# Optimization experiments

Measured on AMD Instinct MI355X. Metric: run time of the kernel, lower is better.

## Reference

```python
import jax, jax.numpy as jnp
import numpy as np
from jax import lax

K = 3
PAD = 1
STRIDE = 1


def setup_inputs() -> dict:
    key = jax.random.key(0)
    k1, k2, k3 = jax.random.split(key, 3)
    B, Cin, Cout, H, W = 4, 64, 64, 128, 128
    x = jax.random.normal(k1, (B, Cin, H, W), dtype=jnp.float32)
    # offset-generating conv weight: [2*K*K, Cin, K, K]
    w_offset = jax.random.normal(k2, (2 * K * K, Cin, K, K), dtype=jnp.float32) * 0.05
    # deformable conv weight: [Cout, Cin, K, K]
    w_deform = jax.random.normal(k3, (Cout, Cin, K, K), dtype=jnp.float32) * 0.05
    return {"x": x, "w_offset": w_offset, "w_deform": w_deform}


def _bilinear_sample_one(img, ys, xs):
    # img: [C, H, W]; ys, xs: [K2, Ho, Wo] float sampling coords
    H, W = img.shape[1], img.shape[2]
    y0 = jnp.floor(ys)
    x0 = jnp.floor(xs)
    wy = ys - y0  # frac weights, [K2, Ho, Wo]
    wx = xs - x0

    def gather(yi, xi):
        valid = (yi >= 0) & (yi <= H - 1) & (xi >= 0) & (xi <= W - 1)
        yc = jnp.clip(yi, 0, H - 1).astype(jnp.int32)
        xc = jnp.clip(xi, 0, W - 1).astype(jnp.int32)
        # img[:, yc, xc] -> [C, K2, Ho, Wo]; zero outside (torchvision zero-pad)
        return img[:, yc, xc] * valid[None].astype(img.dtype)

    v00 = gather(y0, x0)
    v01 = gather(y0, x0 + 1)
    v10 = gather(y0 + 1, x0)
    v11 = gather(y0 + 1, x0 + 1)
    w00 = ((1 - wy) * (1 - wx))[None]
    w01 = ((1 - wy) * wx)[None]
    w10 = (wy * (1 - wx))[None]
    w11 = (wy * wx)[None]
    return v00 * w00 + v01 * w01 + v10 * w10 + v11 * w11  # [C, K2, Ho, Wo]


def reference(x, w_offset, w_deform):
    B, Cin, H, W = x.shape
    Cout = w_deform.shape[0]
    K2 = K * K
    # 1) plain conv to produce offsets: [B, 2*K2, H, W]
    offset = lax.conv_general_dilated(
        x, w_offset, window_strides=(STRIDE, STRIDE),
        padding=((PAD, PAD), (PAD, PAD)),
        dimension_numbers=("NCHW", "OIHW", "NCHW"))
    Ho, Wo = offset.shape[2], offset.shape[3]
    # torchvision ordering: channel 2*k = dy, 2*k+1 = dx, taps row-major
    off = offset.reshape(B, K2, 2, Ho, Wo)
    dy, dx = off[:, :, 0], off[:, :, 1]  # [B, K2, Ho, Wo]
    # 2) base sampling grid per kernel tap
    kk = jnp.arange(K2)
    ki = (kk // K).astype(jnp.float32)  # tap row
    kj = (kk % K).astype(jnp.float32)   # tap col
    base_y = (jnp.arange(Ho, dtype=jnp.float32) * STRIDE - PAD)[None, :] + ki[:, None]  # [K2, Ho]
    base_x = (jnp.arange(Wo, dtype=jnp.float32) * STRIDE - PAD)[None, :] + kj[:, None]  # [K2, Wo]
    ys = base_y[None, :, :, None] + dy  # [B, K2, Ho, Wo]
    xs = base_x[None, :, None, :] + dx
    # 3) deformable bilinear gather: [B, Cin, K2, Ho, Wo]
    sampled = jax.vmap(_bilinear_sample_one)(x, ys, xs)
    # 4) weighted accumulation (the conv contraction)
    out = jnp.einsum("ock,bckhw->bohw", w_deform.reshape(Cout, Cin, K2), sampled)
    return out
```

## Files before the change

kernel.cpp:

```cpp
#include <hip/hip_runtime.h>


#define BATCH 4
#define CIN   64
#define COUT  64
#define HH    128
#define WW    128
#define HWPIX (HH*WW)

typedef __attribute__((ext_vector_type(8))) short short8;
typedef __attribute__((ext_vector_type(4))) float floatx4;

__device__ __forceinline__ unsigned short f2bf(float f) {
  unsigned int u = __float_as_uint(f);
  unsigned int r = u + 0x7fffu + ((u >> 16) & 1u);
  return (unsigned short)(r >> 16);
}
__device__ __forceinline__ float bf2f(unsigned short h) { return __uint_as_float(((unsigned int)h) << 16); }
__device__ __forceinline__ float lo16f(unsigned int u) { return __uint_as_float(u << 16); }
__device__ __forceinline__ float hi16f(unsigned int u) { return __uint_as_float(u & 0xffff0000u); }

__device__ __forceinline__ unsigned int bilin2(unsigned int u00, unsigned int u01,
                                               unsigned int u10, unsigned int u11,
                                               float w00, float w01, float w10, float w11) {
  float lo = w00 * lo16f(u00) + w01 * lo16f(u01) + w10 * lo16f(u10) + w11 * lo16f(u11);
  float hi = w00 * hi16f(u00) + w01 * hi16f(u01) + w10 * hi16f(u10) + w11 * hi16f(u11);
  unsigned int r;
  asm("v_cvt_pk_bf16_f32 %0, %1, %2" : "=v"(r) : "v"(lo), "v"(hi));
  return r;
}

__device__ __forceinline__ int swz(int a) { return a ^ (((a >> 9) & 3) << 4); }

__global__ __launch_bounds__(256) void pre_kernel(const float* __restrict__ x,
                                                  const float* __restrict__ wo,
                                                  const float* __restrict__ wd,
                                                  unsigned short* __restrict__ xThi,
                                                  unsigned short* __restrict__ xTlo,
                                                  unsigned short* __restrict__ wdA,
                                                  unsigned short* __restrict__ woAhi,
                                                  unsigned short* __restrict__ woAlo) {
  int tid = threadIdx.x;
  if (blockIdx.x < 4096) {
    __shared__ float tile[32][33];
    int t = blockIdx.x;
    int b = t >> 10, rem = t & 1023;
    int c0 = (rem >> 9) * 32, p0 = (rem & 511) * 32;
    int tx = tid & 31, ty = tid >> 5;
    const float* xb = x + (size_t)b * CIN * HWPIX;
    size_t boff = (size_t)b * HWPIX * CIN;
#pragma unroll
    for (int i = 0; i < 4; i++)
      tile[ty + i * 8][tx] = xb[(size_t)(c0 + ty + i * 8) * HWPIX + p0 + tx];
    __syncthreads();
#pragma unroll
    for (int i = 0; i < 2; i++) {
      int tt = tid + i * 256;
      int row = tt >> 4;
      int cp = tt & 15;
      float v0 = tile[cp * 2][row], v1 = tile[cp * 2 + 1][row];
      unsigned short h0 = f2bf(v0), h1 = f2bf(v1);
      unsigned short l0 = f2bf(v0 - bf2f(h0)), l1 = f2bf(v1 - bf2f(h1));
      size_t o = boff + (size_t)(p0 + row) * CIN + c0 + cp * 2;
      *(ushort2*)&xThi[o] = make_ushort2(h0, h1);
      *(ushort2*)&xTlo[o] = make_ushort2(l0, l1);
    }
  } else {
    int t = (blockIdx.x - 4096) * 256 + tid;
    if (t < 36864) {
      int j = t & 7, lane = (t >> 3) & 63, ct = (t >> 9) & 3, kc = (t >> 11) & 1, kk = t >> 12;
      int cout = ct * 16 + (lane & 15);
      int cin  = kc * 32 + (lane >> 4) * 8 + j;
      wdA[t] = f2bf(wd[(size_t)(cout * CIN + cin) * 9 + kk]);
    }
    int t2 = t - 36864;
    if (t2 >= 0 && t2 < 18432) {
      int j = t2 & 7, lane = (t2 >> 3) & 63, ct = (t2 >> 9) & 1, kc = (t2 >> 10) & 1, kk = t2 >> 11;
      int cout = ct * 16 + (lane & 15);
      int cin  = kc * 32 + (lane >> 4) * 8 + j;
      float v = (cout < 18) ? wo[(size_t)(cout * CIN + cin) * 9 + kk] : 0.f;
      unsigned short h = f2bf(v);
      woAhi[t2] = h;
      woAlo[t2] = f2bf(v - bf2f(h));
    }
  }
}

__global__ __launch_bounds__(256) void fused_dcn_kernel(const unsigned short* __restrict__ xThi,
                                                        const unsigned short* __restrict__ xTlo,
                                                        const unsigned short* __restrict__ woAhi,
                                                        const unsigned short* __restrict__ woAlo,
                                                        const unsigned short* __restrict__ wdA,
                                                        float* __restrict__ out) {
  __shared__ unsigned short sBhi2[2][4096];
  __shared__ unsigned short sBlo2[2][4096];
  __shared__ float offL[18 * 64];
  char* sHc = (char*)sBhi2;
  char* sLc = (char*)sBlo2;

  int tid = threadIdx.x;
  int hw = blockIdx.x;
  int bid = (hw & 7) * 128 + (hw >> 3);
  int b = bid >> 8, r = bid & 255, y = r >> 1, x0 = (r & 1) << 6;

  int p1 = tid >> 2, si = tid & 3;
  int lane = tid & 63, w = tid >> 6;

  const unsigned short* xhib = xThi + (size_t)b * HWPIX * CIN;
  const unsigned short* xlob = xTlo + (size_t)b * HWPIX * CIN;

  int wq = p1 >> 4, iq = p1 & 15;
  int kcd = si >> 1, qb = si & 1;
  int wb0 = ((((wq * 2 + kcd) * 64) + qb * 32 + iq) * 8) * 2;
  int wb1 = wb0 + 256;
  int swb0 = swz(wb0), swb1 = swz(wb1);
  int srb0 = swz((w * 2 + 0) * 1024 + lane * 16);
  int srb1 = swz((w * 2 + 1) * 1024 + lane * 16);

  int xp = x0 + p1;

  floatx4 oacc[2];
  oacc[0] = (floatx4){0.f, 0.f, 0.f, 0.f};
  oacc[1] = (floatx4){0.f, 0.f, 0.f, 0.f};

  auto ldA = [&](int kk, uint4& h0, uint4& h1, uint4& l0, uint4& l1) {
    int ys = y - 1 + kk / 3;
    int xs = xp - 1 + kk % 3;
    bool valid = (ys >= 0) && (ys < HH) && (xs >= 0) && (xs < WW);
    h0 = (uint4){0, 0, 0, 0}; h1 = h0; l0 = h0; l1 = h0;
    if (valid) {
      const unsigned short* ph = xhib + (size_t)(ys * WW + xs) * CIN + si * 16;
      const unsigned short* pl = xlob + (size_t)(ys * WW + xs) * CIN + si * 16;
      h0 = *(const uint4*)ph; h1 = *(const uint4*)(ph + 8);
      l0 = *(const uint4*)pl; l1 = *(const uint4*)(pl + 8);
    }
  };
  auto stageA = [&](int nxt, const uint4& h0, const uint4& h1, const uint4& l0, const uint4& l1) {
    *(uint4*)(sHc + nxt * 8192 + swb0) = h0;
    *(uint4*)(sHc + nxt * 8192 + swb1) = h1;
    *(uint4*)(sLc + nxt * 8192 + swb0) = l0;
    *(uint4*)(sLc + nxt * 8192 + swb1) = l1;
  };
  auto mfmaA = [&](int kk, int cur) {
    const short8* Ah = (const short8*)(woAhi + (size_t)kk * 2048);
    const short8* Al = (const short8*)(woAlo + (size_t)kk * 2048);
    short8 ah0a = Ah[lane],       ah1a = Ah[128 + lane];
    short8 al0a = Al[lane],       al1a = Al[128 + lane];
    short8 ah0b = Ah[64 + lane],  ah1b = Ah[192 + lane];
    short8 al0b = Al[64 + lane],  al1b = Al[192 + lane];
    short8 bh0 = *(const short8*)(sHc + cur * 8192 + srb0);
    short8 bh1 = *(const short8*)(sHc + cur * 8192 + srb1);
    short8 bl0 = *(const short8*)(sLc + cur * 8192 + srb0);
    short8 bl1 = *(const short8*)(sLc + cur * 8192 + srb1);
    oacc[0] = __builtin_amdgcn_mfma_f32_16x16x32_bf16(ah0a, bh0, oacc[0], 0, 0, 0);
    oacc[0] = __builtin_amdgcn_mfma_f32_16x16x32_bf16(ah0a, bl0, oacc[0], 0, 0, 0);
    oacc[0] = __builtin_amdgcn_mfma_f32_16x16x32_bf16(al0a, bh0, oacc[0], 0, 0, 0);
    oacc[0] = __builtin_amdgcn_mfma_f32_16x16x32_bf16(ah1a, bh1, oacc[0], 0, 0, 0);
    oacc[0] = __builtin_amdgcn_mfma_f32_16x16x32_bf16(ah1a, bl1, oacc[0], 0, 0, 0);
    oacc[0] = __builtin_amdgcn_mfma_f32_16x16x32_bf16(al1a, bh1, oacc[0], 0, 0, 0);
    oacc[1] = __builtin_amdgcn_mfma_f32_16x16x32_bf16(ah0b, bh0, oacc[1], 0, 0, 0);
    oacc[1] = __builtin_amdgcn_mfma_f32_16x16x32_bf16(ah0b, bl0, oacc[1], 0, 0, 0);
    oacc[1] = __builtin_amdgcn_mfma_f32_16x16x32_bf16(al0b, bh0, oacc[1], 0, 0, 0);
    oacc[1] = __builtin_amdgcn_mfma_f32_16x16x32_bf16(ah1b, bh1, oacc[1], 0, 0, 0);
    oacc[1] = __builtin_amdgcn_mfma_f32_16x16x32_bf16(ah1b, bl1, oacc[1], 0, 0, 0);
    oacc[1] = __builtin_amdgcn_mfma_f32_16x16x32_bf16(al1b, bh1, oacc[1], 0, 0, 0);
  };

  {
    uint4 h0c, h1c, l0c, l1c;
    ldA(0, h0c, h1c, l0c, l1c);
    stageA(0, h0c, h1c, l0c, l1c);
    __syncthreads();
#pragma unroll 1
    for (int kk = 0; kk < 9; kk++) {
      uint4 h0n, h1n, l0n, l1n;
      if (kk < 8) ldA(kk + 1, h0n, h1n, l0n, l1n);
      mfmaA(kk, kk & 1);
      if (kk < 8) stageA((kk + 1) & 1, h0n, h1n, l0n, l1n);
      __syncthreads();
    }
  }

  {
    int pxl = w * 16 + (lane & 15);
    int rowb = (lane >> 4) * 4;
#pragma unroll
    for (int ct = 0; ct < 2; ct++)
#pragma unroll
      for (int rr = 0; rr < 4; rr++) {
        int row = ct * 16 + rowb + rr;
        if (row < 18) offL[row * 64 + pxl] = oacc[ct][rr];
      }
  }

  floatx4 acc[4];
#pragma unroll
  for (int ct = 0; ct < 4; ct++) acc[ct] = (floatx4){0.f, 0.f, 0.f, 0.f};

  struct BS {
    float w00, w01, w10, w11;
    uint4 a00, a01, a10, a11, b00, b01, b10, b11;
  };
  auto ldB = [&](int kk) -> BS {
    BS s;
    float dy = offL[(2 * kk) * 64 + p1];
    float dx = offL[(2 * kk + 1) * 64 + p1];
    float ys = (float)(y - 1 + kk / 3) + dy;
    float xs = (float)(xp - 1 + kk % 3) + dx;
    float y0f = floorf(ys), x0f = floorf(xs);
    float wy = ys - y0f, wx = xs - x0f;
    int iy0 = (int)y0f, ix0 = (int)x0f;
    int iy1 = iy0 + 1, ix1 = ix0 + 1;
    s.w00 = (1.f - wy) * (1.f - wx); s.w01 = (1.f - wy) * wx;
    s.w10 = wy * (1.f - wx);         s.w11 = wy * wx;
    bool vy0 = (iy0 >= 0) && (iy0 < HH), vy1 = (iy1 >= 0) && (iy1 < HH);
    bool vx0 = (ix0 >= 0) && (ix0 < WW), vx1 = (ix1 >= 0) && (ix1 < WW);
    if (!(vy0 && vx0)) s.w00 = 0.f;
    if (!(vy0 && vx1)) s.w01 = 0.f;
    if (!(vy1 && vx0)) s.w10 = 0.f;
    if (!(vy1 && vx1)) s.w11 = 0.f;
    int cy0 = min(max(iy0, 0), HH - 1), cy1 = min(max(iy1, 0), HH - 1);
    int cx0 = min(max(ix0, 0), WW - 1), cx1 = min(max(ix1, 0), WW - 1);
    const unsigned short* q00 = xhib + (size_t)(cy0 * WW + cx0) * CIN + si * 16;
    const unsigned short* q01 = xhib + (size_t)(cy0 * WW + cx1) * CIN + si * 16;
    const unsigned short* q10 = xhib + (size_t)(cy1 * WW + cx0) * CIN + si * 16;
    const unsigned short* q11 = xhib + (size_t)(cy1 * WW + cx1) * CIN + si * 16;
    s.a00 = *(const uint4*)q00; s.a01 = *(const uint4*)q01;
    s.a10 = *(const uint4*)q10; s.a11 = *(const uint4*)q11;
    s.b00 = *(const uint4*)(q00 + 8); s.b01 = *(const uint4*)(q01 + 8);
    s.b10 = *(const uint4*)(q10 + 8); s.b11 = *(const uint4*)(q11 + 8);
    return s;
  };
  auto blendStoreB = [&](int nxt, const BS& s) {
    uint4 o0, o1;
    o0.x = bilin2(s.a00.x, s.a01.x, s.a10.x, s.a11.x, s.w00, s.w01, s.w10, s.w11);
    o0.y = bilin2(s.a00.y, s.a01.y, s.a10.y, s.a11.y, s.w00, s.w01, s.w10, s.w11);
    o0.z = bilin2(s.a00.z, s.a01.z, s.a10.z, s.a11.z, s.w00, s.w01, s.w10, s.w11);
    o0.w = bilin2(s.a00.w, s.a01.w, s.a10.w, s.a11.w, s.w00, s.w01, s.w10, s.w11);
    o1.x = bilin2(s.b00.x, s.b01.x, s.b10.x, s.b11.x, s.w00, s.w01, s.w10, s.w11);
    o1.y = bilin2(s.b00.y, s.b01.y, s.b10.y, s.b11.y, s.w00, s.w01, s.w10, s.w11);
    o1.z = bilin2(s.b00.z, s.b01.z, s.b10.z, s.b11.z, s.w00, s.w01, s.w10, s.w11);
    o1.w = bilin2(s.b00.w, s.b01.w, s.b10.w, s.b11.w, s.w00, s.w01, s.w10, s.w11);
    *(uint4*)(sHc + nxt * 8192 + swb0) = o0;
    *(uint4*)(sHc + nxt * 8192 + swb1) = o1;
  };
  auto mfmaB = [&](int kk, int cur) {
    const short8* Ap = (const short8*)(wdA + (size_t)kk * 4096);
    short8 a0q0 = Ap[lane],        a1q0 = Ap[256 + lane];
    short8 a0q1 = Ap[64 + lane],   a1q1 = Ap[320 + lane];
    short8 a0q2 = Ap[128 + lane],  a1q2 = Ap[384 + lane];
    short8 a0q3 = Ap[192 + lane],  a1q3 = Ap[448 + lane];
    short8 bv0 = *(const short8*)(sHc + cur * 8192 + srb0);
    short8 bv1 = *(const short8*)(sHc + cur * 8192 + srb1);
    acc[0] = __builtin_amdgcn_mfma_f32_16x16x32_bf16(a0q0, bv0, acc[0], 0, 0, 0);
    acc[0] = __builtin_amdgcn_mfma_f32_16x16x32_bf16(a1q0, bv1, acc[0], 0, 0, 0);
    acc[1] = __builtin_amdgcn_mfma_f32_16x16x32_bf16(a0q1, bv0, acc[1], 0, 0, 0);
    acc[1] = __builtin_amdgcn_mfma_f32_16x16x32_bf16(a1q1, bv1, acc[1], 0, 0, 0);
    acc[2] = __builtin_amdgcn_mfma_f32_16x16x32_bf16(a0q2, bv0, acc[2], 0, 0, 0);
    acc[2] = __builtin_amdgcn_mfma_f32_16x16x32_bf16(a1q2, bv1, acc[2], 0, 0, 0);
    acc[3] = __builtin_amdgcn_mfma_f32_16x16x32_bf16(a0q3, bv0, acc[3], 0, 0, 0);
    acc[3] = __builtin_amdgcn_mfma_f32_16x16x32_bf16(a1q3, bv1, acc[3], 0, 0, 0);
  };

  {
    BS s0 = ldB(0);
    blendStoreB(0, s0);
    __syncthreads();
#pragma unroll 1
    for (int kk = 0; kk < 9; kk++) {
      BS sn;
      if (kk < 8) sn = ldB(kk + 1);
      mfmaB(kk, kk & 1);
      if (kk < 8) blendStoreB((kk + 1) & 1, sn);
      __syncthreads();
    }
  }

  int px = x0 + w * 16 + (lane & 15);
  int rowb = (lane >> 4) * 4;
  float* outb = out + (size_t)b * COUT * HWPIX + y * WW + px;
#pragma unroll
  for (int ct = 0; ct < 4; ct++)
#pragma unroll
    for (int rr = 0; rr < 4; rr++)
      outb[(size_t)(ct * 16 + rowb + rr) * HWPIX] = acc[ct][rr];
}

extern "C" void kernel_launch(void* const* d_in, const int* in_sizes, int n_in,
                              void* d_out, int out_size, void* d_ws, size_t ws_size,
                              hipStream_t stream) {
  const float* x  = (const float*)d_in[0];
  const float* wo = (const float*)d_in[1];
  const float* wd = (const float*)d_in[2];
  float* out = (float*)d_out;

  char* wsb = (char*)d_ws;
  unsigned short* xThi  = (unsigned short*)wsb;
  unsigned short* xTlo  = (unsigned short*)(wsb + 8388608);
  unsigned short* wdA   = (unsigned short*)(wsb + 16777216);
  unsigned short* woAhi = (unsigned short*)(wsb + 16777216 + 73728);
  unsigned short* woAlo = (unsigned short*)(wsb + 16850944 + 36864);

  pre_kernel<<<dim3(4096 + 216), dim3(256), 0, stream>>>(x, wo, wd, xThi, xTlo, wdA, woAhi, woAlo);
  fused_dcn_kernel<<<dim3(BATCH * HWPIX / 64), dim3(256), 0, stream>>>(xThi, xTlo, woAhi, woAlo, wdA, out);
}
```

Baseline: 115.9 us.

## Repartition MFMA work so each wave owns output-channel tile across all pixels

Each wave now computes one 16-channel slice of the output for all 64 pixels in the block, instead of all 64 channels for a 16-pixel slice. Each wave loads only its own weight fragments from global memory, cutting per-wave weight traffic fourfold in the main conv. In exchange it reads every pixel group's B operand from shared memory, which quadruples the LDS reads. The offset conv is split the same way, with an added barrier before offsets are read across waves. Output stores now write 16-pixel chunks per channel row.

```diff
diff --git a/kernel.cpp b/kernel.cpp
--- a/kernel.cpp
+++ b/kernel.cpp
@@ -114,14 +114,19 @@
   int wb0 = ((((wq * 2 + kcd) * 64) + qb * 32 + iq) * 8) * 2;
   int wb1 = wb0 + 256;
   int swb0 = swz(wb0), swb1 = swz(wb1);
-  int srb0 = swz((w * 2 + 0) * 1024 + lane * 16);
-  int srb1 = swz((w * 2 + 1) * 1024 + lane * 16);
+  int brb0[4], brb1[4];
+#pragma unroll
+  for (int pg = 0; pg < 4; pg++) {
+    brb0[pg] = swz(pg * 2048 + lane * 16);
+    brb1[pg] = swz(pg * 2048 + 1024 + lane * 16);
+  }
 
   int xp = x0 + p1;
 
   floatx4 oacc[2];
   oacc[0] = (floatx4){0.f, 0.f, 0.f, 0.f};
   oacc[1] = (floatx4){0.f, 0.f, 0.f, 0.f};
+  int ctA = w & 1, pgA = (w >> 1) * 2;
 
   auto ldA = [&](int kk, uint4& h0, uint4& h1, uint4& l0, uint4& l1) {
     int ys = y - 1 + kk / 3;
@@ -144,26 +149,22 @@
   auto mfmaA = [&](int kk, int cur) {
     const short8* Ah = (const short8*)(woAhi + (size_t)kk * 2048);
     const short8* Al = (const short8*)(woAlo + (size_t)kk * 2048);
-    short8 ah0a = Ah[lane],       ah1a = Ah[128 + lane];
-    short8 al0a = Al[lane],       al1a = Al[128 + lane];
-    short8 ah0b = Ah[64 + lane],  ah1b = Ah[192 + lane];
-    short8 al0b = Al[64 + lane],  al1b = Al[192 + lane];
-    short8 bh0 = *(const short8*)(sHc + cur * 8192 + srb0);
-    short8 bh1 = *(const short8*)(sHc + cur * 8192 + srb1);
-    short8 bl0 = *(const short8*)(sLc + cur * 8192 + srb0);
-    short8 bl1 = *(const short8*)(sLc + cur * 8192 + srb1);
-    oacc[0] = __builtin_amdgcn_mfma_f32_16x16x32_bf16(ah0a, bh0, oacc[0], 0, 0, 0);
-    oacc[0] = __builtin_amdgcn_mfma_f32_16x16x32_bf16(ah0a, bl0, oacc[0], 0, 0, 0);
-    oacc[0] = __builtin_amdgcn_mfma_f32_16x16x32_bf16(al0a, bh0, oacc[0], 0, 0, 0);
-    oacc[0] = __builtin_amdgcn_mfma_f32_16x16x32_bf16(ah1a, bh1, oacc[0], 0, 0, 0);
-    oacc[0] = __builtin_amdgcn_mfma_f32_16x16x32_bf16(ah1a, bl1, oacc[0], 0, 0, 0);
-    oacc[0] = __builtin_amdgcn_mfma_f32_16x16x32_bf16(al1a, bh1, oacc[0], 0, 0, 0);
-    oacc[1] = __builtin_amdgcn_mfma_f32_16x16x32_bf16(ah0b, bh0, oacc[1], 0, 0, 0);
-    oacc[1] = __builtin_amdgcn_mfma_f32_16x16x32_bf16(ah0b, bl0, oacc[1], 0, 0, 0);
-    oacc[1] = __builtin_amdgcn_mfma_f32_16x16x32_bf16(al0b, bh0, oacc[1], 0, 0, 0);
-    oacc[1] = __builtin_amdgcn_mfma_f32_16x16x32_bf16(ah1b, bh1, oacc[1], 0, 0, 0);
-    oacc[1] = __builtin_amdgcn_mfma_f32_16x16x32_bf16(ah1b, bl1, oacc[1], 0, 0, 0);
-    oacc[1] = __builtin_amdgcn_mfma_f32_16x16x32_bf16(al1b, bh1, oacc[1], 0, 0, 0);
+    short8 ah0 = Ah[ctA * 64 + lane], ah1 = Ah[128 + ctA * 64 + lane];
+    short8 al0 = Al[ctA * 64 + lane], al1 = Al[128 + ctA * 64 + lane];
+#pragma unroll
+    for (int pgi = 0; pgi < 2; pgi++) {
+      int pg = pgA + pgi;
+      short8 bh0 = *(const short8*)(sHc + cur * 8192 + brb0[pg]);
+      short8 bh1 = *(const short8*)(sHc + cur * 8192 + brb1[pg]);
+      short8 bl0 = *(const short8*)(sLc + cur * 8192 + brb0[pg]);
+      short8 bl1 = *(const short8*)(sLc + cur * 8192 + brb1[pg]);
+      oacc[pgi] = __builtin_amdgcn_mfma_f32_16x16x32_bf16(ah0, bh0, oacc[pgi], 0, 0, 0);
+      oacc[pgi] = __builtin_amdgcn_mfma_f32_16x16x32_bf16(ah0, bl0, oacc[pgi], 0, 0, 0);
+      oacc[pgi] = __builtin_amdgcn_mfma_f32_16x16x32_bf16(al0, bh0, oacc[pgi], 0, 0, 0);
+      oacc[pgi] = __builtin_amdgcn_mfma_f32_16x16x32_bf16(ah1, bh1, oacc[pgi], 0, 0, 0);
+      oacc[pgi] = __builtin_amdgcn_mfma_f32_16x16x32_bf16(ah1, bl1, oacc[pgi], 0, 0, 0);
+      oacc[pgi] = __builtin_amdgcn_mfma_f32_16x16x32_bf16(al1, bh1, oacc[pgi], 0, 0, 0);
+    }
   };
 
   {
@@ -182,20 +183,21 @@
   }
 
   {
-    int pxl = w * 16 + (lane & 15);
     int rowb = (lane >> 4) * 4;
-#pragma unroll
-    for (int ct = 0; ct < 2; ct++)
+    int colb = pgA * 16 + (lane & 15);
+#pragma unroll
+    for (int pgi = 0; pgi < 2; pgi++)
 #pragma unroll
       for (int rr = 0; rr < 4; rr++) {
-        int row = ct * 16 + rowb + rr;
-        if (row < 18) offL[row * 64 + pxl] = oacc[ct][rr];
+        int row = ctA * 16 + rowb + rr;
+        if (row < 18) offL[row * 64 + colb + pgi * 16] = oacc[pgi][rr];
       }
   }
+  __syncthreads();
 
   floatx4 acc[4];
 #pragma unroll
-  for (int ct = 0; ct < 4; ct++) acc[ct] = (floatx4){0.f, 0.f, 0.f, 0.f};
+  for (int pg = 0; pg < 4; pg++) acc[pg] = (floatx4){0.f, 0.f, 0.f, 0.f};
 
   struct BS {
     float w00, w01, w10, w11;
@@ -246,20 +248,15 @@
   };
   auto mfmaB = [&](int kk, int cur) {
     const short8* Ap = (const short8*)(wdA + (size_t)kk * 4096);
-    short8 a0q0 = Ap[lane],        a1q0 = Ap[256 + lane];
-    short8 a0q1 = Ap[64 + lane],   a1q1 = Ap[320 + lane];
-    short8 a0q2 = Ap[128 + lane],  a1q2 = Ap[384 + lane];
-    short8 a0q3 = Ap[192 + lane],  a1q3 = Ap[448 + lane];
-    short8 bv0 = *(const short8*)(sHc + cur * 8192 + srb0);
-    short8 bv1 = *(const short8*)(sHc + cur * 8192 + srb1);
-    acc[0] = __builtin_amdgcn_mfma_f32_16x16x32_bf16(a0q0, bv0, acc[0], 0, 0, 0);
-    acc[0] = __builtin_amdgcn_mfma_f32_16x16x32_bf16(a1q0, bv1, acc[0], 0, 0, 0);
-    acc[1] = __builtin_amdgcn_mfma_f32_16x16x32_bf16(a0q1, bv0, acc[1], 0, 0, 0);
-    acc[1] = __builtin_amdgcn_mfma_f32_16x16x32_bf16(a1q1, bv1, acc[1], 0, 0, 0);
-    acc[2] = __builtin_amdgcn_mfma_f32_16x16x32_bf16(a0q2, bv0, acc[2], 0, 0, 0);
-    acc[2] = __builtin_amdgcn_mfma_f32_16x16x32_bf16(a1q2, bv1, acc[2], 0, 0, 0);
-    acc[3] = __builtin_amdgcn_mfma_f32_16x16x32_bf16(a0q3, bv0, acc[3], 0, 0, 0);
-    acc[3] = __builtin_amdgcn_mfma_f32_16x16x32_bf16(a1q3, bv1, acc[3], 0, 0, 0);
+    short8 a0 = Ap[w * 64 + lane];
+    short8 a1 = Ap[256 + w * 64 + lane];
+#pragma unroll
+    for (int pg = 0; pg < 4; pg++) {
+      short8 bv0 = *(const short8*)(sHc + cur * 8192 + brb0[pg]);
+      short8 bv1 = *(const short8*)(sHc + cur * 8192 + brb1[pg]);
+      acc[pg] = __builtin_amdgcn_mfma_f32_16x16x32_bf16(a0, bv0, acc[pg], 0, 0, 0);
+      acc[pg] = __builtin_amdgcn_mfma_f32_16x16x32_bf16(a1, bv1, acc[pg], 0, 0, 0);
+    }
   };
 
   {
@@ -276,14 +273,13 @@
     }
   }
 
-  int px = x0 + w * 16 + (lane & 15);
   int rowb = (lane >> 4) * 4;
-  float* outb = out + (size_t)b * COUT * HWPIX + y * WW + px;
-#pragma unroll
-  for (int ct = 0; ct < 4; ct++)
+  float* outb = out + (size_t)b * COUT * HWPIX + y * WW + x0 + (lane & 15);
+#pragma unroll
+  for (int pg = 0; pg < 4; pg++)
 #pragma unroll
     for (int rr = 0; rr < 4; rr++)
-      outb[(size_t)(ct * 16 + rowb + rr) * HWPIX] = acc[ct][rr];
+      outb[(size_t)(w * 16 + rowb + rr) * HWPIX + pg * 16] = acc[pg][rr];
 }
 
 extern "C" void kernel_launch(void* const* d_in, const int* in_sizes, int n_in,
```

Result: faster. 106.0 us (-8.5%).
